# Kernel optimization log

Measured on AMD Instinct MI355X. Metric: run time of the kernel, lower is better.

The kernel has to match this reference:

```python
import jax, jax.numpy as jnp
import numpy as np

BETA = 0.25
N_E = 256
E_DIM = 1024


def setup_inputs() -> dict:
    key = jax.random.key(0)
    k1, k2, k3, k4 = jax.random.split(key, 4)
    z = jax.random.normal(k1, (16, E_DIM, 32, 32), dtype=jnp.float32)
    emb = jax.random.normal(k2, (N_E, E_DIM), dtype=jnp.float32)
    conv_w = jax.random.normal(k3, (E_DIM, E_DIM), dtype=jnp.float32) * 0.02
    conv_b = jax.random.normal(k4, (E_DIM,), dtype=jnp.float32) * 0.02
    return {"z": z, "emb": emb, "conv_w": conv_w, "conv_b": conv_b}


def reference(z, emb, conv_w, conv_b):
    # z: [B, C=e_dim, H, W] -> channels-last, flatten spatial+batch
    zp = jnp.transpose(z, (0, 2, 3, 1))          # [B, H, W, C]
    zf = zp.reshape(-1, E_DIM)                    # [N, C]
    # squared L2 distances to codebook: [N, n_e]
    d = (jnp.sum(zf * zf, axis=1, keepdims=True)
         + jnp.sum(emb * emb, axis=1)
         - 2.0 * (zf @ emb.T))
    min_idx = jnp.argmin(d, axis=1)               # [N]
    min_enc = jax.nn.one_hot(min_idx, N_E, dtype=z.dtype)  # [N, n_e]
    z_q = (min_enc @ emb).reshape(zp.shape)       # gather via matmul, as original
    # VQ commitment loss with straight-through estimator
    loss = (jnp.mean((jax.lax.stop_gradient(z_q) - zp) ** 2)
            + BETA * jnp.mean((z_q - jax.lax.stop_gradient(zp)) ** 2))
    z_q = zp + jax.lax.stop_gradient(z_q - zp)
    e_mean = jnp.mean(min_enc, axis=0)
    perplexity = jnp.exp(-jnp.sum(e_mean * jnp.log(e_mean + 1e-10)))
    # back to channels-first, then 1x1 conv (= per-pixel GEMM)
    z_q = jnp.transpose(z_q, (0, 3, 1, 2))        # [B, C, H, W]
    out = jnp.einsum('bchw,oc->bohw', z_q, conv_w) + conv_b[None, :, None, None]
    return out, loss, perplexity, min_idx
```

## Files before the change

kernel.cpp:

```cpp
#include <hip/hip_runtime.h>
#include <math.h>

#define NE 256
#define EDIM 1024
#define HW 1024
#define NPIX 16384
#define OUT_ELEMS 16777216

typedef short short8 __attribute__((ext_vector_type(8)));
typedef float f32x4 __attribute__((ext_vector_type(4)));

#define WS_HIST   0
#define WS_LOSS   1024
#define WS_ZSQ    1028
#define WS_FBITS  2048
#define WS_T      4096
#define WS_MEMSET 1052672
#define WS_ZERO_N4 65792
#define WS_CE2    1052672
#define WS_IDX    1053696
#define WS_EH     1119232
#define WS_EL     1643520
#define WS_NEED   2167808

#define DELTA 0.02f

#define WO_CE2  0
#define WO_HIST 1024
#define WO_LOSS 2048
#define WO_IDX  4096
#define WO_T    69632
#define WO_TOTAL 1118208

__device__ __forceinline__ unsigned short f2bf(float f) {
    unsigned u = __float_as_uint(f);
    unsigned r = u + 0x7FFFu + ((u >> 16) & 1u);
    return (unsigned short)(r >> 16);
}
__device__ __forceinline__ float bf2f(unsigned short h) {
    return __uint_as_float(((unsigned)h) << 16);
}

__device__ __forceinline__ void stage16(const void* g, void* l) {
    __builtin_amdgcn_global_load_lds(
        (const __attribute__((address_space(1))) unsigned int*)g,
        (__attribute__((address_space(3))) unsigned int*)l, 16, 0, 0);
}

__global__ __launch_bounds__(64) void k_prep(const float* __restrict__ emb,
                                             unsigned short* __restrict__ eh,
                                             unsigned short* __restrict__ el,
                                             float* __restrict__ ce2,
                                             float4* __restrict__ zws) {
    int j = blockIdx.x;
    int l = threadIdx.x;
    for (int i = j * 64 + l; i < WS_ZERO_N4; i += 256 * 64)
        zws[i] = (float4){0.f, 0.f, 0.f, 0.f};
    const float* row = emb + ((size_t)j << 10);
    float s = 0.f;
    #pragma unroll
    for (int i = 0; i < 4; i++) {
        float4 v = *(const float4*)(row + l * 4 + 256 * i);
        s += v.x * v.x + v.y * v.y + v.z * v.z + v.w * v.w;
        unsigned short h0 = f2bf(v.x), h1 = f2bf(v.y), h2 = f2bf(v.z), h3 = f2bf(v.w);
        uint2 hp, lp;
        hp.x = (unsigned)h0 | ((unsigned)h1 << 16);
        hp.y = (unsigned)h2 | ((unsigned)h3 << 16);
        lp.x = (unsigned)f2bf(v.x - bf2f(h0)) | ((unsigned)f2bf(v.y - bf2f(h1)) << 16);
        lp.y = (unsigned)f2bf(v.z - bf2f(h2)) | ((unsigned)f2bf(v.w - bf2f(h3)) << 16);
        *(uint2*)(eh + ((size_t)j << 10) + l * 4 + 256 * i) = hp;
        *(uint2*)(el + ((size_t)j << 10) + l * 4 + 256 * i) = lp;
    }
    #pragma unroll
    for (int m = 32; m; m >>= 1) s += __shfl_down(s, m, 64);
    if (l == 0) ce2[j] = 0.5f * s;
}

__global__ __launch_bounds__(256) void k_wT(const float* __restrict__ w,
                                            const float* __restrict__ emb,
                                            float* __restrict__ T) {
    __shared__ float wt[64 * 17];
    __shared__ float et[64 * 17];
    int t = threadIdx.x;
    int j0 = blockIdx.x * 64;
    int o0 = blockIdx.y * 64;
    int kb = blockIdx.z * 256;
    int to = t & 15, tj = t >> 4;
    float acc[4][4] = {};
    int lr = t >> 2, lk = (t & 3) * 4;
    for (int kk = kb; kk < kb + 256; kk += 16) {
        float4 wv = *(const float4*)(w + (size_t)(o0 + lr) * EDIM + kk + lk);
        float4 ev = *(const float4*)(emb + (size_t)(j0 + lr) * EDIM + kk + lk);
        __syncthreads();
        wt[lr * 17 + lk + 0] = wv.x; wt[lr * 17 + lk + 1] = wv.y;
        wt[lr * 17 + lk + 2] = wv.z; wt[lr * 17 + lk + 3] = wv.w;
        et[lr * 17 + lk + 0] = ev.x; et[lr * 17 + lk + 1] = ev.y;
        et[lr * 17 + lk + 2] = ev.z; et[lr * 17 + lk + 3] = ev.w;
        __syncthreads();
        #pragma unroll
        for (int k = 0; k < 16; k++) {
            float a[4], b[4];
            #pragma unroll
            for (int i = 0; i < 4; i++) a[i] = wt[(to * 4 + i) * 17 + k];
            #pragma unroll
            for (int i = 0; i < 4; i++) b[i] = et[(tj * 4 + i) * 17 + k];
            #pragma unroll
            for (int i = 0; i < 4; i++)
                #pragma unroll
                for (int jx = 0; jx < 4; jx++) acc[i][jx] += a[i] * b[jx];
        }
    }
    #pragma unroll
    for (int i = 0; i < 4; i++)
        #pragma unroll
        for (int jx = 0; jx < 4; jx++)
            atomicAdd(&T[(size_t)(o0 + to * 4 + i) * NE + j0 + tj * 4 + jx],
                      acc[i][jx]);
}

__global__ __launch_bounds__(256) void k_dist(
        const float* __restrict__ z, const unsigned short* __restrict__ eh,
        const unsigned short* __restrict__ el,
        const float* __restrict__ ce2,
        int* __restrict__ idx_i, float* __restrict__ idx_f,
        int* __restrict__ hist, float* __restrict__ loss_s,
        float* __restrict__ zsq_acc, unsigned int* __restrict__ fbits) {
    __shared__ unsigned short sB[4][2][256 * 32];
    int t = threadIdx.x;
    int lane = t & 63, w = t >> 6;
    int m = lane & 15, quad = lane >> 4;
    int px0 = blockIdx.x * 64;
    int b = px0 >> 10;
    const float* zp = z + (((size_t)b) << 20) + (px0 & 1023) + w * 16 + m;
    int sc = t >> 2, qp = t & 3;
    int ql = qp ^ ((sc >> 1) & 3);

    f32x4 acc[16];
    #pragma unroll
    for (int nt = 0; nt < 16; nt++) acc[nt] = (f32x4){0.f, 0.f, 0.f, 0.f};

    float zv0[8], zv1[8], zv2[8], zv3[8];
    float zsq = 0.f;
    int sq = quad ^ ((m >> 1) & 3);

#define STAGE(c, B) do {                                                        \
    int kk_ = (c) * 32;                                                         \
    _Pragma("unroll")                                                           \
    for (int i_ = 0; i_ < 4; i_++) {                                            \
        stage16(eh + (((size_t)(i_ * 64 + sc)) << 10) + kk_ + ql * 8,           \
                &sB[B][0][(i_ * 256 + w * 64) * 8]);                            \
        stage16(el + (((size_t)(i_ * 64 + sc)) << 10) + kk_ + ql * 8,           \
                &sB[B][1][(i_ * 256 + w * 64) * 8]);                            \
    } } while (0)

#define ZLOAD(c, ZV) do {                                                       \
    int kk_ = (c) * 32;                                                         \
    _Pragma("unroll")                                                           \
    for (int j_ = 0; j_ < 8; j_++)                                              \
        ZV[j_] = zp[((size_t)(kk_ + quad * 8 + j_)) << 10];                     \
    } while (0)

#define WAITV(n) do {                                                           \
    asm volatile("s_waitcnt vmcnt(" #n ")" ::: "memory");                       \
    __builtin_amdgcn_sched_barrier(0); } while (0)

#define FENCE() do {                                                            \
    asm volatile("" ::: "memory");                                              \
    __builtin_amdgcn_sched_barrier(0); } while (0)

#define BODY(c, B, ZV, PRE, B3, ZV3) do {                                       \
    __builtin_amdgcn_s_barrier();                                               \
    short8 ah, al;                                                              \
    _Pragma("unroll")                                                           \
    for (int j_ = 0; j_ < 8; j_++) {                                            \
        float zj_ = ZV[j_];                                                     \
        zsq += zj_ * zj_;                                                       \
        unsigned short h_ = f2bf(zj_);                                          \
        ((unsigned short*)&ah)[j_] = h_;                                        \
        ((unsigned short*)&al)[j_] = f2bf(zj_ - bf2f(h_));                      \
    }                                                                           \
    if (PRE) { STAGE((c) + 3, B3); ZLOAD((c) + 3, ZV3); }                       \
    _Pragma("unroll")                                                           \
    for (int nt_ = 0; nt_ < 16; nt_++) {                                        \
        short8 bh_ = *(const short8*)&sB[B][0][(nt_ * 16 + m) * 32 + sq * 8];   \
        short8 bl_ = *(const short8*)&sB[B][1][(nt_ * 16 + m) * 32 + sq * 8];   \
        acc[nt_] = __builtin_amdgcn_mfma_f32_16x16x32_bf16(ah, bh_, acc[nt_], 0, 0, 0); \
        acc[nt_] = __builtin_amdgcn_mfma_f32_16x16x32_bf16(ah, bl_, acc[nt_], 0, 0, 0); \
        acc[nt_] = __builtin_amdgcn_mfma_f32_16x16x32_bf16(al, bh_, acc[nt_], 0, 0, 0); \
    } } while (0)

    STAGE(0, 0); ZLOAD(0, zv0); FENCE();
    STAGE(1, 1); ZLOAD(1, zv1); FENCE();
    STAGE(2, 2); ZLOAD(2, zv2);

    for (int mi = 0; mi < 7; mi++) {
        WAITV(32); BODY(mi * 4 + 0, 0, zv0, 1, 3, zv3);
        WAITV(32); BODY(mi * 4 + 1, 1, zv1, 1, 0, zv0);
        WAITV(32); BODY(mi * 4 + 2, 2, zv2, 1, 1, zv1);
        WAITV(32); BODY(mi * 4 + 3, 3, zv3, 1, 2, zv2);
    }
    WAITV(32); BODY(28, 0, zv0, 1, 3, zv3);
    WAITV(32); BODY(29, 1, zv1, 0, 2, zv2);
    WAITV(16); BODY(30, 2, zv2, 0, 3, zv3);
    WAITV(0);  BODY(31, 3, zv3, 0, 0, zv0);

#undef STAGE
#undef ZLOAD
#undef WAITV
#undef FENCE
#undef BODY

    #pragma unroll
    for (int msk = 32; msk; msk >>= 1) zsq += __shfl_down(zsq, msk, 64);
    if (lane == 0) atomicAdd(zsq_acc, zsq);

    float c2v[16];
    #pragma unroll
    for (int nt = 0; nt < 16; nt++) c2v[nt] = ce2[nt * 16 + m];

    float lsum = 0.f;
    #pragma unroll
    for (int r = 0; r < 4; r++) {
        float v1 = 3.4e38f, v2 = 3.4e38f; int i1 = 0;
        #pragma unroll
        for (int nt = 0; nt < 16; nt++) {
            int code = nt * 16 + m;
            float sv = c2v[nt] - acc[nt][r];
            if (sv < v1 || (sv == v1 && code < i1)) { v2 = v1; v1 = sv; i1 = code; }
            else v2 = fminf(v2, sv);
        }
        #pragma unroll
        for (int msk = 1; msk < 16; msk <<= 1) {
            float ov1 = __shfl_xor(v1, msk, 64);
            int   oi1 = __shfl_xor(i1, msk, 64);
            float ov2 = __shfl_xor(v2, msk, 64);
            float nv2 = fminf(fminf(v2, ov2), fmaxf(v1, ov1));
            if (ov1 < v1 || (ov1 == v1 && oi1 < i1)) { v1 = ov1; i1 = oi1; }
            v2 = nv2;
        }
        if (m == 0) {
            int px = px0 + w * 16 + quad * 4 + r;
            idx_i[px] = i1;
            idx_f[px] = (float)i1;
            atomicAdd(&hist[i1], 1);
            if (v2 - v1 < DELTA)
                atomicOr(&fbits[px >> 5], 1u << (px & 31));
            lsum += v1;
        }
    }
    lsum += __shfl_xor(lsum, 16, 64);
    lsum += __shfl_xor(lsum, 32, 64);
    if (lane == 0) atomicAdd(loss_s, lsum);
}

__global__ __launch_bounds__(256) void k_cleanup(const float* __restrict__ z,
        const float* __restrict__ emb, const float* __restrict__ ce2,
        const unsigned int* __restrict__ fbits,
        int* __restrict__ idx_i, float* __restrict__ idx_f, int* __restrict__ hist) {
    __shared__ float zs[1024];
    __shared__ float rv[4];
    __shared__ int ri[4];
    int t = threadIdx.x;
    const float* er = emb + (size_t)t * EDIM;
    for (int px = blockIdx.x; px < NPIX; px += gridDim.x) {
        if (!(fbits[px >> 5] & (1u << (px & 31)))) continue;
        int b = px >> 10, p = px & 1023;
        const float* zb = z + (((size_t)b) << 20) + p;
        #pragma unroll
        for (int r = 0; r < 4; r++) {
            int c = t + 256 * r;
            zs[c] = zb[((size_t)c) << 10];
        }
        __syncthreads();
        float d0 = 0.f, d1 = 0.f, d2 = 0.f, d3 = 0.f;
        #pragma unroll 4
        for (int c = 0; c < EDIM; c += 16) {
            float4 e0 = *(const float4*)(er + c);
            float4 e1 = *(const float4*)(er + c + 4);
            float4 e2 = *(const float4*)(er + c + 8);
            float4 e3 = *(const float4*)(er + c + 12);
            d0 += e0.x * zs[c]      + e0.y * zs[c + 1]  + e0.z * zs[c + 2]  + e0.w * zs[c + 3];
            d1 += e1.x * zs[c + 4]  + e1.y * zs[c + 5]  + e1.z * zs[c + 6]  + e1.w * zs[c + 7];
            d2 += e2.x * zs[c + 8]  + e2.y * zs[c + 9]  + e2.z * zs[c + 10] + e2.w * zs[c + 11];
            d3 += e3.x * zs[c + 12] + e3.y * zs[c + 13] + e3.z * zs[c + 14] + e3.w * zs[c + 15];
        }
        float sv = ce2[t] - ((d0 + d1) + (d2 + d3));
        int bi = t;
        #pragma unroll
        for (int msk = 1; msk < 64; msk <<= 1) {
            float ov = __shfl_xor(sv, msk, 64);
            int oi = __shfl_xor(bi, msk, 64);
            if (ov < sv || (ov == sv && oi < bi)) { sv = ov; bi = oi; }
        }
        if ((t & 63) == 0) { rv[t >> 6] = sv; ri[t >> 6] = bi; }
        __syncthreads();
        if (t == 0) {
            float v = rv[0]; int ix = ri[0];
            for (int ww = 1; ww < 4; ww++)
                if (rv[ww] < v || (rv[ww] == v && ri[ww] < ix)) { v = rv[ww]; ix = ri[ww]; }
            int old = idx_i[px];
            if (ix != old) {
                idx_i[px] = ix; idx_f[px] = (float)ix;
                atomicAdd(&hist[ix], 1); atomicSub(&hist[old], 1);
            }
        }
        __syncthreads();
    }
}

__global__ __launch_bounds__(64) void k_norms(const float* __restrict__ emb,
                                              float* __restrict__ ce2) {
    int j = blockIdx.x;
    int lane = threadIdx.x;
    const float* row = emb + (size_t)j * EDIM;
    float s = 0.f;
    #pragma unroll
    for (int i = 0; i < EDIM / 64; i++) {
        float v = row[lane + 64 * i];
        s += v * v;
    }
    #pragma unroll
    for (int m = 32; m; m >>= 1) s += __shfl_down(s, m, 64);
    if (lane == 0) ce2[j] = 0.5f * s;
}

__global__ __launch_bounds__(256) void k_argmin(const float* __restrict__ z,
                                                const float* __restrict__ emb,
                                                const float* __restrict__ ce2,
                                                int* __restrict__ idx_i,
                                                float* __restrict__ idx_f,
                                                int* __restrict__ hist,
                                                float* __restrict__ loss_acc) {
    __shared__ float zt[32 * 64];
    __shared__ float et[256 * 34];
    __shared__ float znorm_s[64];
    int t = threadIdx.x;
    int n0 = blockIdx.x * 64;
    int b = n0 >> 10;
    int p0 = n0 & 1023;
    const float* zb = z + (size_t)b * EDIM * HW;
    int tc = t & 31, tp = t >> 5;
    float acc[8][8] = {};
    float znorm = 0.f;
    for (int kk = 0; kk < EDIM; kk += 32) {
        #pragma unroll
        for (int i = 0; i < 16; i++) {
            int q = t + 256 * i;
            int code = q >> 4, k2 = q & 15;
            float2 v = *(const float2*)(emb + (size_t)code * EDIM + kk + k2 * 2);
            *(float2*)(et + code * 34 + k2 * 2) = v;
        }
        #pragma unroll
        for (int i = 0; i < 4; i++) {
            int q = t + 256 * i;
            int k = q >> 5, p2 = q & 31;
            float2 v = *(const float2*)(zb + (size_t)(kk + k) * HW + p0 + p2 * 2);
            *(float2*)(zt + k * 64 + p2 * 2) = v;
        }
        __syncthreads();
        if (t < 64) {
            #pragma unroll
            for (int k = 0; k < 32; k++) { float zz = zt[k * 64 + t]; znorm += zz * zz; }
        }
        #pragma unroll 4
        for (int k2 = 0; k2 < 16; k2++) {
            float2 ev[8], za[4], zb2[4];
            #pragma unroll
            for (int u = 0; u < 8; u++)
                ev[u] = *(float2*)(et + (tc + 32 * u) * 34 + k2 * 2);
            #pragma unroll
            for (int j = 0; j < 4; j++)
                za[j] = *(float2*)(zt + (2 * k2) * 64 + tp * 8 + 2 * j);
            #pragma unroll
            for (int j = 0; j < 4; j++)
                zb2[j] = *(float2*)(zt + (2 * k2 + 1) * 64 + tp * 8 + 2 * j);
            #pragma unroll
            for (int p = 0; p < 8; p++) {
                float z0 = (p & 1) ? za[p >> 1].y : za[p >> 1].x;
                float z1 = (p & 1) ? zb2[p >> 1].y : zb2[p >> 1].x;
                #pragma unroll
                for (int u = 0; u < 8; u++)
                    acc[p][u] += z0 * ev[u].x + z1 * ev[u].y;
            }
        }
        __syncthreads();
    }
    if (t < 64) znorm_s[t] = znorm;
    float minv[8];
    int mini[8];
    #pragma unroll
    for (int p = 0; p < 8; p++) { minv[p] = 3.4e38f; mini[p] = 0; }
    #pragma unroll
    for (int u = 0; u < 8; u++) {
        int code = tc + 32 * u;
        float cc2 = ce2[code];
        #pragma unroll
        for (int p = 0; p < 8; p++) {
            float s = cc2 - acc[p][u];
            if (s < minv[p] || (s == minv[p] && code < mini[p])) { minv[p] = s; mini[p] = code; }
        }
    }
    #pragma unroll
    for (int m = 1; m < 32; m <<= 1) {
        #pragma unroll
        for (int p = 0; p < 8; p++) {
            float ov = __shfl_xor(minv[p], m, 64);
            int oi = __shfl_xor(mini[p], m, 64);
            if (ov < minv[p] || (ov == minv[p] && oi < mini[p])) { minv[p] = ov; mini[p] = oi; }
        }
    }
    __syncthreads();
    if (tc == 0) {
        float dsum = 0.f;
        #pragma unroll
        for (int p = 0; p < 8; p++) {
            int lp = tp * 8 + p;
            int n = n0 + lp;
            idx_i[n] = mini[p];
            idx_f[n] = (float)mini[p];
            dsum += znorm_s[lp] + 2.f * minv[p];
            atomicAdd(&hist[mini[p]], 1);
        }
        atomicAdd(loss_acc, dsum);
    }
}

__global__ __launch_bounds__(256) void k_scatter_f(const float* __restrict__ T,
                                                   const float* __restrict__ bias,
                                                   const int* __restrict__ idx,
                                                   const int* __restrict__ hist,
                                                   const float* __restrict__ loss_s,
                                                   const float* __restrict__ zsq,
                                                   float* __restrict__ out) {
    __shared__ float Ts[16 * 256];
    __shared__ float bs[16];
    __shared__ float red[4];
    int t = threadIdx.x;
    int o0 = blockIdx.x * 16;
    int b = blockIdx.y;
    #pragma unroll
    for (int r = 0; r < 16; r++)
        Ts[r * 256 + t] = T[(size_t)(o0 + r) * NE + t];
    if (t < 16) bs[t] = bias[o0 + t];
    __syncthreads();
    int4 i4 = *(const int4*)(idx + b * HW + t * 4);
    #pragma unroll
    for (int r = 0; r < 16; r++) {
        const float* Tr = Ts + r * 256;
        float bb = bs[r];
        float4 v;
        v.x = Tr[i4.x] + bb;
        v.y = Tr[i4.y] + bb;
        v.z = Tr[i4.z] + bb;
        v.w = Tr[i4.w] + bb;
        *(float4*)(out + ((size_t)(b * EDIM + o0 + r) * HW) + t * 4) = v;
    }
    if (blockIdx.x == 0 && blockIdx.y == 0) {
        float em = (float)hist[t] * (1.0f / 16384.0f);
        float v = em * logf(em + 1e-10f);
        #pragma unroll
        for (int m = 32; m; m >>= 1) v += __shfl_down(v, m, 64);
        if ((t & 63) == 0) red[t >> 6] = v;
        __syncthreads();
        if (t == 0) {
            float s = red[0] + red[1] + red[2] + red[3];
            out[OUT_ELEMS] = (zsq[0] + 2.f * loss_s[0]) * 1.25f / 16777216.f;
            out[OUT_ELEMS + 1] = expf(-s);
        }
    }
}

__global__ __launch_bounds__(256) void k_scatter(const float* __restrict__ T,
                                                 const float* __restrict__ bias,
                                                 const int* __restrict__ idx,
                                                 float* __restrict__ out) {
    __shared__ float Ts[16 * 256];
    __shared__ float bs[16];
    int t = threadIdx.x;
    int o0 = blockIdx.x * 16;
    int b = blockIdx.y;
    #pragma unroll
    for (int r = 0; r < 16; r++)
        Ts[r * 256 + t] = T[(size_t)(o0 + r) * NE + t];
    if (t < 16) bs[t] = bias[o0 + t];
    __syncthreads();
    int4 i4 = *(const int4*)(idx + b * HW + t * 4);
    #pragma unroll
    for (int r = 0; r < 16; r++) {
        const float* Tr = Ts + r * 256;
        float bb = bs[r];
        float4 v;
        v.x = Tr[i4.x] + bb;
        v.y = Tr[i4.y] + bb;
        v.z = Tr[i4.z] + bb;
        v.w = Tr[i4.w] + bb;
        *(float4*)(out + ((size_t)(b * EDIM + o0 + r) * HW) + t * 4) = v;
    }
}

__global__ __launch_bounds__(256) void k_final_old(const int* __restrict__ hist,
                                                   const float* __restrict__ loss_acc,
                                                   float* __restrict__ out) {
    __shared__ float red[4];
    int t = threadIdx.x;
    float em = (float)hist[t] * (1.0f / 16384.0f);
    float v = em * logf(em + 1e-10f);
    #pragma unroll
    for (int m = 32; m; m >>= 1) v += __shfl_down(v, m, 64);
    if ((t & 63) == 0) red[t >> 6] = v;
    __syncthreads();
    if (t == 0) {
        float s = red[0] + red[1] + red[2] + red[3];
        out[OUT_ELEMS] = loss_acc[0] * 1.25f / 16777216.f;
        out[OUT_ELEMS + 1] = expf(-s);
    }
}

extern "C" void kernel_launch(void* const* d_in, const int* in_sizes, int n_in,
                              void* d_out, int out_size, void* d_ws, size_t ws_size,
                              hipStream_t stream) {
    (void)in_sizes; (void)n_in; (void)out_size;
    const float* z      = (const float*)d_in[0];
    const float* emb    = (const float*)d_in[1];
    const float* conv_w = (const float*)d_in[2];
    const float* conv_b = (const float*)d_in[3];
    float* out = (float*)d_out;

    if (ws_size >= WS_NEED) {
        int*   hist     = (int*)((char*)d_ws + WS_HIST);
        float* loss_s   = (float*)((char*)d_ws + WS_LOSS);
        float* zsq      = (float*)((char*)d_ws + WS_ZSQ);
        unsigned int* fbits = (unsigned int*)((char*)d_ws + WS_FBITS);
        float* T        = (float*)((char*)d_ws + WS_T);
        float* ce2      = (float*)((char*)d_ws + WS_CE2);
        int*   idx_i    = (int*)((char*)d_ws + WS_IDX);
        unsigned short* eh = (unsigned short*)((char*)d_ws + WS_EH);
        unsigned short* el = (unsigned short*)((char*)d_ws + WS_EL);
        float* idx_f = out + OUT_ELEMS + 2;

        k_prep<<<NE, 64, 0, stream>>>(emb, eh, el, ce2, (float4*)d_ws);
        k_wT<<<dim3(4, 16, 4), 256, 0, stream>>>(conv_w, emb, T);
        k_dist<<<256, 256, 0, stream>>>(z, eh, el, ce2, idx_i, idx_f,
                                        hist, loss_s, zsq, fbits);
        k_cleanup<<<256, 256, 0, stream>>>(z, emb, ce2, fbits, idx_i, idx_f, hist);
        k_scatter_f<<<dim3(64, 16), 256, 0, stream>>>(T, conv_b, idx_i,
                                                      hist, loss_s, zsq, out);
    } else {
        float* ce2      = (float*)((char*)d_ws + WO_CE2);
        int*   hist     = (int*)((char*)d_ws + WO_HIST);
        float* loss_acc = (float*)((char*)d_ws + WO_LOSS);
        int*   idx_i    = (int*)((char*)d_ws + WO_IDX);
        float* T        = (float*)((char*)d_ws + WO_T);
        float* idx_f = out + OUT_ELEMS + 2;

        hipMemsetAsync(d_ws, 0, WO_TOTAL, stream);
        k_norms<<<NE, 64, 0, stream>>>(emb, ce2);
        k_wT<<<dim3(4, 16, 4), 256, 0, stream>>>(conv_w, emb, T);
        k_argmin<<<256, 256, 0, stream>>>(z, emb, ce2, idx_i, idx_f, hist, loss_acc);
        k_scatter<<<dim3(64, 16), 256, 0, stream>>>(T, conv_b, idx_i, out);
        k_final_old<<<1, 256, 0, stream>>>(hist, loss_acc, out);
    }
}
```

Baseline: 249.4 us.

## Split k_dist codebook across wave pairs with 512-thread blocks

k_dist now runs 8 waves per block instead of 4. Each pair of waves covers the same 16 pixels but only half of the 256 codes, which halves the accumulator registers per wave, and the staging loads are spread across all 8 waves. The two halves' argmin results (best, second-best, index) are merged through shared memory after a block barrier. This aims to raise latency hiding and MFMA issue parallelism on a 256-block grid, at the cost of each wave converting and loading z redundantly and one extra sync.

```diff
diff --git a/kernel.cpp b/kernel.cpp
--- a/kernel.cpp
+++ b/kernel.cpp
@@ -118,7 +118,7 @@
                       acc[i][jx]);
 }
 
-__global__ __launch_bounds__(256) void k_dist(
+__global__ __launch_bounds__(512) void k_dist(
         const float* __restrict__ z, const unsigned short* __restrict__ eh,
         const unsigned short* __restrict__ el,
         const float* __restrict__ ce2,
@@ -126,18 +126,22 @@
         int* __restrict__ hist, float* __restrict__ loss_s,
         float* __restrict__ zsq_acc, unsigned int* __restrict__ fbits) {
     __shared__ unsigned short sB[4][2][256 * 32];
+    __shared__ float v1h[64], v2h[64];
+    __shared__ int   i1h[64];
     int t = threadIdx.x;
     int lane = t & 63, w = t >> 6;
     int m = lane & 15, quad = lane >> 4;
+    int pt = w >> 1, ch = w & 1;
+    int c_base = ch << 7;
     int px0 = blockIdx.x * 64;
     int b = px0 >> 10;
-    const float* zp = z + (((size_t)b) << 20) + (px0 & 1023) + w * 16 + m;
-    int sc = t >> 2, qp = t & 3;
-    int ql = qp ^ ((sc >> 1) & 3);
-
-    f32x4 acc[16];
-    #pragma unroll
-    for (int nt = 0; nt < 16; nt++) acc[nt] = (f32x4){0.f, 0.f, 0.f, 0.f};
+    const float* zp = z + (((size_t)b) << 20) + (px0 & 1023) + pt * 16 + m;
+    int sr0 = w * 32 + (lane >> 2);
+    int qsl = (lane & 3) ^ ((sr0 >> 1) & 3);
+
+    f32x4 acc[8];
+    #pragma unroll
+    for (int nt = 0; nt < 8; nt++) acc[nt] = (f32x4){0.f, 0.f, 0.f, 0.f};
 
     float zv0[8], zv1[8], zv2[8], zv3[8];
     float zsq = 0.f;
@@ -145,13 +149,15 @@
 
 #define STAGE(c, B) do {                                                        \
     int kk_ = (c) * 32;                                                         \
-    _Pragma("unroll")                                                           \
-    for (int i_ = 0; i_ < 4; i_++) {                                            \
-        stage16(eh + (((size_t)(i_ * 64 + sc)) << 10) + kk_ + ql * 8,           \
-                &sB[B][0][(i_ * 256 + w * 64) * 8]);                            \
-        stage16(el + (((size_t)(i_ * 64 + sc)) << 10) + kk_ + ql * 8,           \
-                &sB[B][1][(i_ * 256 + w * 64) * 8]);                            \
-    } } while (0)
+    stage16(eh + (((size_t)sr0) << 10) + kk_ + qsl * 8,                         \
+            &sB[B][0][(w * 2) * 64 * 8]);                                       \
+    stage16(el + (((size_t)sr0) << 10) + kk_ + qsl * 8,                         \
+            &sB[B][1][(w * 2) * 64 * 8]);                                       \
+    stage16(eh + (((size_t)(sr0 + 16)) << 10) + kk_ + qsl * 8,                  \
+            &sB[B][0][(w * 2 + 1) * 64 * 8]);                                   \
+    stage16(el + (((size_t)(sr0 + 16)) << 10) + kk_ + qsl * 8,                  \
+            &sB[B][1][(w * 2 + 1) * 64 * 8]);                                   \
+    } while (0)
 
 #define ZLOAD(c, ZV) do {                                                       \
     int kk_ = (c) * 32;                                                         \
@@ -181,9 +187,10 @@
     }                                                                           \
     if (PRE) { STAGE((c) + 3, B3); ZLOAD((c) + 3, ZV3); }                       \
     _Pragma("unroll")                                                           \
-    for (int nt_ = 0; nt_ < 16; nt_++) {                                        \
-        short8 bh_ = *(const short8*)&sB[B][0][(nt_ * 16 + m) * 32 + sq * 8];   \
-        short8 bl_ = *(const short8*)&sB[B][1][(nt_ * 16 + m) * 32 + sq * 8];   \
+    for (int nt_ = 0; nt_ < 8; nt_++) {                                         \
+        int crow_ = (c_base + nt_ * 16 + m) * 32;                               \
+        short8 bh_ = *(const short8*)&sB[B][0][crow_ + sq * 8];                 \
+        short8 bl_ = *(const short8*)&sB[B][1][crow_ + sq * 8];                 \
         acc[nt_] = __builtin_amdgcn_mfma_f32_16x16x32_bf16(ah, bh_, acc[nt_], 0, 0, 0); \
         acc[nt_] = __builtin_amdgcn_mfma_f32_16x16x32_bf16(ah, bl_, acc[nt_], 0, 0, 0); \
         acc[nt_] = __builtin_amdgcn_mfma_f32_16x16x32_bf16(al, bh_, acc[nt_], 0, 0, 0); \
@@ -194,14 +201,14 @@
     STAGE(2, 2); ZLOAD(2, zv2);
 
     for (int mi = 0; mi < 7; mi++) {
-        WAITV(32); BODY(mi * 4 + 0, 0, zv0, 1, 3, zv3);
-        WAITV(32); BODY(mi * 4 + 1, 1, zv1, 1, 0, zv0);
-        WAITV(32); BODY(mi * 4 + 2, 2, zv2, 1, 1, zv1);
-        WAITV(32); BODY(mi * 4 + 3, 3, zv3, 1, 2, zv2);
-    }
-    WAITV(32); BODY(28, 0, zv0, 1, 3, zv3);
-    WAITV(32); BODY(29, 1, zv1, 0, 2, zv2);
-    WAITV(16); BODY(30, 2, zv2, 0, 3, zv3);
+        WAITV(24); BODY(mi * 4 + 0, 0, zv0, 1, 3, zv3);
+        WAITV(24); BODY(mi * 4 + 1, 1, zv1, 1, 0, zv0);
+        WAITV(24); BODY(mi * 4 + 2, 2, zv2, 1, 1, zv1);
+        WAITV(24); BODY(mi * 4 + 3, 3, zv3, 1, 2, zv2);
+    }
+    WAITV(24); BODY(28, 0, zv0, 1, 3, zv3);
+    WAITV(24); BODY(29, 1, zv1, 0, 2, zv2);
+    WAITV(12); BODY(30, 2, zv2, 0, 3, zv3);
     WAITV(0);  BODY(31, 3, zv3, 0, 0, zv0);
 
 #undef STAGE
@@ -212,19 +219,20 @@
 
     #pragma unroll
     for (int msk = 32; msk; msk >>= 1) zsq += __shfl_down(zsq, msk, 64);
-    if (lane == 0) atomicAdd(zsq_acc, zsq);
-
-    float c2v[16];
-    #pragma unroll
-    for (int nt = 0; nt < 16; nt++) c2v[nt] = ce2[nt * 16 + m];
-
-    float lsum = 0.f;
+    if (ch == 0 && lane == 0) atomicAdd(zsq_acc, zsq);
+
+    float c2v[8];
+    #pragma unroll
+    for (int nt = 0; nt < 8; nt++) c2v[nt] = ce2[c_base + nt * 16 + m];
+
+    float v1r[4], v2r[4];
+    int i1r[4];
     #pragma unroll
     for (int r = 0; r < 4; r++) {
         float v1 = 3.4e38f, v2 = 3.4e38f; int i1 = 0;
         #pragma unroll
-        for (int nt = 0; nt < 16; nt++) {
-            int code = nt * 16 + m;
+        for (int nt = 0; nt < 8; nt++) {
+            int code = c_base + nt * 16 + m;
             float sv = c2v[nt] - acc[nt][r];
             if (sv < v1 || (sv == v1 && code < i1)) { v2 = v1; v1 = sv; i1 = code; }
             else v2 = fminf(v2, sv);
@@ -238,19 +246,42 @@
             if (ov1 < v1 || (ov1 == v1 && oi1 < i1)) { v1 = ov1; i1 = oi1; }
             v2 = nv2;
         }
+        v1r[r] = v1; v2r[r] = v2; i1r[r] = i1;
+    }
+    int pxl = pt * 16 + quad * 4;
+    if (ch == 0 && m == 0) {
+        #pragma unroll
+        for (int r = 0; r < 4; r++) {
+            v1h[pxl + r] = v1r[r]; v2h[pxl + r] = v2r[r]; i1h[pxl + r] = i1r[r];
+        }
+    }
+    __syncthreads();
+    if (ch == 1) {
+        float lsum = 0.f;
         if (m == 0) {
-            int px = px0 + w * 16 + quad * 4 + r;
-            idx_i[px] = i1;
-            idx_f[px] = (float)i1;
-            atomicAdd(&hist[i1], 1);
-            if (v2 - v1 < DELTA)
-                atomicOr(&fbits[px >> 5], 1u << (px & 31));
-            lsum += v1;
-        }
-    }
-    lsum += __shfl_xor(lsum, 16, 64);
-    lsum += __shfl_xor(lsum, 32, 64);
-    if (lane == 0) atomicAdd(loss_s, lsum);
+            #pragma unroll
+            for (int r = 0; r < 4; r++) {
+                int pl = pxl + r;
+                float va = v1h[pl], v2a = v2h[pl];
+                int   ia = i1h[pl];
+                float vb = v1r[r];
+                float v2m = fminf(fminf(v2a, v2r[r]), fmaxf(va, vb));
+                float v1; int i1;
+                if (vb < va) { v1 = vb; i1 = i1r[r]; }
+                else         { v1 = va; i1 = ia; }
+                int px = px0 + pl;
+                idx_i[px] = i1;
+                idx_f[px] = (float)i1;
+                atomicAdd(&hist[i1], 1);
+                if (v2m - v1 < DELTA)
+                    atomicOr(&fbits[px >> 5], 1u << (px & 31));
+                lsum += v1;
+            }
+        }
+        lsum += __shfl_xor(lsum, 16, 64);
+        lsum += __shfl_xor(lsum, 32, 64);
+        if (lane == 0) atomicAdd(loss_s, lsum);
+    }
 }
 
 __global__ __launch_bounds__(256) void k_cleanup(const float* __restrict__ z,
@@ -540,7 +571,7 @@
 
         k_prep<<<NE, 64, 0, stream>>>(emb, eh, el, ce2, (float4*)d_ws);
         k_wT<<<dim3(4, 16, 4), 256, 0, stream>>>(conv_w, emb, T);
-        k_dist<<<256, 256, 0, stream>>>(z, eh, el, ce2, idx_i, idx_f,
+        k_dist<<<256, 512, 0, stream>>>(z, eh, el, ce2, idx_i, idx_f,
                                         hist, loss_s, zsq, fbits);
         k_cleanup<<<256, 256, 0, stream>>>(z, emb, ce2, fbits, idx_i, idx_f, hist);
         k_scatter_f<<<dim3(64, 16), 256, 0, stream>>>(T, conv_b, idx_i,
```

New measurement: 244.2 us. -2.1%, faster.
